# Kernel tuning notes

Hardware: AMD Instinct MI355X
Metric: run time of the kernel (lower is better)

Reference implementation:

```python
import jax, jax.numpy as jnp
import numpy as np

SCALE_FACTOR = 8.0  # sqrt(head_dim=64)
GAMMA = 1.0
NEG_INF = -1e9


def setup_inputs() -> dict:
    key = jax.random.key(0)
    kq, kk, kv, km = jax.random.split(key, 4)
    B, H, S, D = 4, 16, 2048, 64
    q = jax.random.normal(kq, (B, H, S, D), dtype=jnp.float32)
    k = jax.random.normal(kk, (B, H, S, D), dtype=jnp.float32)
    v = jax.random.normal(kv, (B, H, S, D), dtype=jnp.float32)
    mask = jax.random.randint(km, (B, 1, S, S), 0, 2, dtype=jnp.int32)
    return {"q": q, "k": k, "v": v, "mask": mask}


def reference(q, k, v, mask):
    # attn = (q/scale) @ k^T, masked, softmax along last dim, scaled by gamma
    scores = jnp.einsum("bhsd,bhtd->bhst", q / SCALE_FACTOR, k)  # [B,H,S,S]
    scores = jnp.where(mask == 0, NEG_INF, scores)
    attn = jax.nn.softmax(scores, axis=-1) * GAMMA
    output = jnp.einsum("bhst,bhtd->bhsd", attn, v) + v  # AV + residual V
    return (output, attn)
```

## Files before the change

kernel.cpp:

```cpp
#include <hip/hip_runtime.h>

typedef _Float16 f16;
typedef _Float16 f16x4 __attribute__((ext_vector_type(4)));
typedef _Float16 f16x8 __attribute__((ext_vector_type(8)));
typedef float f32x16 __attribute__((ext_vector_type(16)));

#define MFMA16(a, b, c) __builtin_amdgcn_mfma_f32_32x32x16_f16((a), (b), (c), 0, 0, 0)

constexpr int B_ = 4, H_ = 16, S_ = 2048, D_ = 64, BH = 64;
constexpr int QB = 128;
constexpr int WQ = 32;
constexpr int KB = 64;
constexpr int TS = 512;
constexpr int NSPLIT = S_ / TS;
constexpr int NKT_W = TS / KB;
constexpr int NKT = S_ / KB;
constexpr int MW = S_ / 32;
constexpr size_t OUT0 = (size_t)B_ * H_ * S_ * D_;
constexpr size_t WS_RSUM_OFF = (size_t)B_ * S_ * MW;

__device__ __forceinline__ int swzb(int row, int col ) {
  int byte = (row << 7) + (col << 1);
  return byte ^ ((row & 7) << 4);
}

__device__ __forceinline__ void kload256(const float* g, int kt, int tid, float4 kr[4]) {
#pragma unroll
  for (int rep = 0; rep < 4; ++rep) {
    int idx = (rep * 256 + tid) * 4;
    kr[rep] = *(const float4*)(g + (size_t)(kt * KB + (idx >> 6)) * D_ + (idx & 63));
  }
}
__device__ __forceinline__ void kwrite256(char* KlB, int tid, const float4 kr[4]) {
#pragma unroll
  for (int rep = 0; rep < 4; ++rep) {
    int idx = (rep * 256 + tid) * 4;
    f16x4 hx = {(f16)kr[rep].x, (f16)kr[rep].y, (f16)kr[rep].z, (f16)kr[rep].w};
    *(f16x4*)(KlB + swzb(idx >> 6, idx & 63)) = hx;
  }
}
__device__ __forceinline__ void vwrite256(char* VtB, int tid, const float4 vr[4]) {
#pragma unroll
  for (int rep = 0; rep < 4; ++rep) {
    int idx = (rep * 256 + tid) * 4;
    int row = idx >> 6, col = idx & 63;
    *(f16*)(VtB + swzb(col + 0, row)) = (f16)vr[rep].x;
    *(f16*)(VtB + swzb(col + 1, row)) = (f16)vr[rep].y;
    *(f16*)(VtB + swzb(col + 2, row)) = (f16)vr[rep].z;
    *(f16*)(VtB + swzb(col + 3, row)) = (f16)vr[rep].w;
  }
}

__device__ __forceinline__ void load_qf(const float* qg, int qrow, int hi, f16x8 qf[4]) {
  const float* qr = qg + (size_t)qrow * D_;
#pragma unroll
  for (int s = 0; s < 4; ++s) {
    const int d0 = s * 16 + hi * 8;
    float4 a = *(const float4*)(qr + d0);
    float4 c = *(const float4*)(qr + d0 + 4);
    f16x8 t;
    t[0] = (f16)(a.x * 0.125f); t[1] = (f16)(a.y * 0.125f);
    t[2] = (f16)(a.z * 0.125f); t[3] = (f16)(a.w * 0.125f);
    t[4] = (f16)(c.x * 0.125f); t[5] = (f16)(c.y * 0.125f);
    t[6] = (f16)(c.z * 0.125f); t[7] = (f16)(c.w * 0.125f);
    qf[s] = t;
  }
}

__device__ __forceinline__ f32x16 qk8(const char* KlB, const f16x8 qf[4], int sub, int ln, int hi) {
  f32x16 s;
#pragma unroll
  for (int i = 0; i < 16; ++i) s[i] = 0.0f;
#pragma unroll
  for (int t = 0; t < 4; ++t) {
    f16x8 kf = *(const f16x8*)(KlB + swzb(sub * 32 + ln, t * 16 + hi * 8));
    s = MFMA16(qf[t], kf, s);
  }
  return s;
}

__global__ void zero_ws(float* __restrict__ p, int n) {
  int i = blockIdx.x * blockDim.x + threadIdx.x;
  if (i < n) p[i] = 0.0f;
}

__global__ __launch_bounds__(256) void mask_pack(const int* __restrict__ mg,
                                                 unsigned* __restrict__ mb) {
  const int tid = threadIdx.x, lane = tid & 63, wid = tid >> 6;
  const int row = blockIdx.x * 4 + wid;
  const int* mrow = mg + (size_t)row * S_;
  unsigned long long myw = 0;
#pragma unroll
  for (int w = 0; w < 32; ++w) {
    int m = mrow[w * 64 + lane];
    unsigned long long bal = __ballot(m != 0);
    if (lane == w) myw = bal;
  }
  if (lane < 32) *(unsigned long long*)(mb + (size_t)row * MW + 2 * lane) = myw;
}

__global__ __launch_bounds__(256, 4) void attn_rsum(
    const float* __restrict__ qg_, const float* __restrict__ kg_,
    const unsigned* __restrict__ mb, float* __restrict__ ws) {
  __shared__ f16 Kl[KB * D_];
  const int tid = threadIdx.x, lane = tid & 63, wid = tid >> 6;
  const int ln = lane & 31, hi = lane >> 5;
  const int i = blockIdx.x;
  const int work = (i & 7) * 512 + (i >> 3);
  const int bh = work >> 6, rem = work & 63;
  const int qb = (rem & 15) * QB + wid * WQ;
  const int kt0 = (rem >> 4) * NKT_W;
  const int b = bh >> 4;
  const float* qg = qg_ + (size_t)bh * S_ * D_;
  const float* kg = kg_ + (size_t)bh * S_ * D_;
  const unsigned* mbB = mb + (size_t)b * S_ * MW;
  char* KlB = (char*)Kl;

  f16x8 qf[4];
  load_qf(qg, qb + ln, hi, qf);
  float rs[16];
#pragma unroll
  for (int r = 0; r < 16; ++r) rs[r] = 0.0f;

  float4 kr[4];
  kload256(kg, kt0, tid, kr);
  for (int it = 0; it < NKT_W; ++it) {
    __syncthreads();
    kwrite256(KlB, tid, kr);
    if (it + 1 < NKT_W) kload256(kg, kt0 + it + 1, tid, kr);
    __syncthreads();
#pragma unroll
    for (int sub = 0; sub < 2; ++sub) {
      const int t0 = (kt0 + it) * KB + sub * 32;
      f32x16 sacc = qk8(KlB, qf, sub, ln, hi);
#pragma unroll
      for (int r = 0; r < 16; ++r) {
        const int qoff = (r & 3) + 8 * (r >> 2);
        const unsigned mw = mbB[(size_t)(qb + qoff + 4 * hi) * MW + (t0 >> 5)];
        rs[r] += ((mw >> ln) & 1u) ? __expf(sacc[r]) : 0.0f;
      }
    }
  }
  float* wsrow = ws + (size_t)bh * S_;
#pragma unroll
  for (int r = 0; r < 16; ++r) {
    float s = rs[r];
    s += __shfl_xor(s, 16); s += __shfl_xor(s, 8); s += __shfl_xor(s, 4);
    s += __shfl_xor(s, 2); s += __shfl_xor(s, 1);
    if (ln == 0) {
      const int qoff = (r & 3) + 8 * (r >> 2);
      atomicAdd(wsrow + qb + qoff + 4 * hi, s);
    }
  }
}

__global__ __launch_bounds__(256, 4) void attn_emit(
    const float* __restrict__ qg_, const float* __restrict__ kg_,
    const unsigned* __restrict__ mb, const float* __restrict__ ws,
    float* __restrict__ out) {
  __shared__ f16 Kl[KB * D_];
  const int tid = threadIdx.x, lane = tid & 63, wid = tid >> 6;
  const int ln = lane & 31, hi = lane >> 5;
  const int i = blockIdx.x;
  const int work = (i & 7) * 512 + (i >> 3);
  const int bh = work >> 6, rem = work & 63;
  const int qb = (rem & 15) * QB + wid * WQ;
  const int kt0 = (rem >> 4) * NKT_W;
  const int b = bh >> 4;
  const float* qg = qg_ + (size_t)bh * S_ * D_;
  const float* kg = kg_ + (size_t)bh * S_ * D_;
  const unsigned* mbB = mb + (size_t)b * S_ * MW;
  float* attnp = out + OUT0 + (size_t)bh * S_ * S_;
  char* KlB = (char*)Kl;

  f16x8 qf[4];
  load_qf(qg, qb + ln, hi, qf);
  const float* wsrow = ws + (size_t)bh * S_;
  float rinv[16];
#pragma unroll
  for (int r = 0; r < 16; ++r) {
    const int qoff = (r & 3) + 8 * (r >> 2);
    rinv[r] = 1.0f / wsrow[qb + qoff + 4 * hi];
  }

  float4 kr[4];
  kload256(kg, kt0, tid, kr);
  for (int it = 0; it < NKT_W; ++it) {
    __syncthreads();
    kwrite256(KlB, tid, kr);
    if (it + 1 < NKT_W) kload256(kg, kt0 + it + 1, tid, kr);
    __syncthreads();
#pragma unroll
    for (int sub = 0; sub < 2; ++sub) {
      const int t0 = (kt0 + it) * KB + sub * 32;
      f32x16 sacc = qk8(KlB, qf, sub, ln, hi);
      float* arow = attnp + (size_t)(qb + 4 * hi) * S_ + t0 + ln;
#pragma unroll
      for (int r = 0; r < 16; ++r) {
        const int qoff = (r & 3) + 8 * (r >> 2);
        const unsigned mw = mbB[(size_t)(qb + qoff + 4 * hi) * MW + (t0 >> 5)];
        float p = ((mw >> ln) & 1u) ? __expf(sacc[r]) * rinv[r] : 0.0f;
        arow[(size_t)qoff * S_] = p;
      }
    }
  }
}

__global__ __launch_bounds__(256) void attn_out(
    const float* __restrict__ qg_, const float* __restrict__ kg_,
    const float* __restrict__ vg_, const unsigned* __restrict__ mb,
    const float* __restrict__ ws, float* __restrict__ out) {
  __shared__ f16 Kl[KB * D_];
  __shared__ f16 Vt[D_ * KB];
  __shared__ f16 Pl[4 * WQ * KB];
  const int tid = threadIdx.x, lane = tid & 63, wid = tid >> 6;
  const int ln = lane & 31, hi = lane >> 5;
  const int i = blockIdx.x;
  const int work = (i & 7) * 128 + (i >> 3);
  const int bh = work >> 4;
  const int qb = (work & 15) * QB + wid * WQ;
  const int b = bh >> 4;
  const float* qg = qg_ + (size_t)bh * S_ * D_;
  const float* kg = kg_ + (size_t)bh * S_ * D_;
  const float* vg = vg_ + (size_t)bh * S_ * D_;
  const unsigned* mbB = mb + (size_t)b * S_ * MW;
  float* outp = out + (size_t)bh * S_ * D_;
  char* KlB = (char*)Kl;
  char* VtB = (char*)Vt;
  char* PlB = (char*)Pl + wid * (WQ * KB * 2);

  f16x8 qf[4];
  load_qf(qg, qb + ln, hi, qf);
  const float* wsrow = ws + (size_t)bh * S_;
  float rinv[16];
#pragma unroll
  for (int r = 0; r < 16; ++r) {
    const int qoff = (r & 3) + 8 * (r >> 2);
    rinv[r] = 1.0f / wsrow[qb + qoff + 4 * hi];
  }

  f32x16 oacc0, oacc1;
#pragma unroll
  for (int i2 = 0; i2 < 16; ++i2) { oacc0[i2] = 0.0f; oacc1[i2] = 0.0f; }

  float4 kr[4], vr[4];
  kload256(kg, 0, tid, kr);
  kload256(vg, 0, tid, vr);
  for (int kt = 0; kt < NKT; ++kt) {
    __syncthreads();
    kwrite256(KlB, tid, kr);
    vwrite256(VtB, tid, vr);
    if (kt + 1 < NKT) {
      kload256(kg, kt + 1, tid, kr);
      kload256(vg, kt + 1, tid, vr);
    }
    __syncthreads();
#pragma unroll
    for (int sub = 0; sub < 2; ++sub) {
      const int t0 = kt * KB + sub * 32;
      f32x16 sacc = qk8(KlB, qf, sub, ln, hi);
#pragma unroll
      for (int r = 0; r < 16; ++r) {
        const int qoff = (r & 3) + 8 * (r >> 2);
        const unsigned mw = mbB[(size_t)(qb + qoff + 4 * hi) * MW + (t0 >> 5)];
        float p = ((mw >> ln) & 1u) ? __expf(sacc[r]) * rinv[r] : 0.0f;
        *(f16*)(PlB + swzb(qoff + 4 * hi, sub * 32 + ln)) = (f16)p;
      }
    }
#pragma unroll
    for (int ts = 0; ts < 4; ++ts) {
      f16x8 pa = *(const f16x8*)(PlB + swzb(ln, ts * 16 + hi * 8));
      f16x8 vb0 = *(const f16x8*)(VtB + swzb(ln, ts * 16 + hi * 8));
      f16x8 vb1 = *(const f16x8*)(VtB + swzb(32 + ln, ts * 16 + hi * 8));
      oacc0 = MFMA16(pa, vb0, oacc0);
      oacc1 = MFMA16(pa, vb1, oacc1);
    }
  }

#pragma unroll
  for (int r = 0; r < 16; ++r) {
    const int qoff = (r & 3) + 8 * (r >> 2);
    const size_t o = (size_t)(qb + qoff + 4 * hi) * D_ + ln;
    outp[o] = oacc0[r] + vg[o];
    outp[o + 32] = oacc1[r] + vg[o + 32];
  }
}

extern "C" void kernel_launch(void* const* d_in, const int* in_sizes, int n_in,
                              void* d_out, int out_size, void* d_ws, size_t ws_size,
                              hipStream_t stream) {
  (void)in_sizes; (void)n_in; (void)out_size; (void)ws_size;
  const float* q = (const float*)d_in[0];
  const float* k = (const float*)d_in[1];
  const float* v = (const float*)d_in[2];
  const int* mask = (const int*)d_in[3];
  float* out = (float*)d_out;
  unsigned* mb = (unsigned*)d_ws;
  float* rs = (float*)d_ws + WS_RSUM_OFF;

  const int nsum = BH * S_;
  zero_ws<<<dim3((nsum + 255) / 256), dim3(256), 0, stream>>>(rs, nsum);
  mask_pack<<<dim3(B_ * S_ / 4), dim3(256), 0, stream>>>(mask, mb);
  attn_rsum<<<dim3(16 * NSPLIT * BH), dim3(256), 0, stream>>>(q, k, mb, rs);
  attn_emit<<<dim3(16 * NSPLIT * BH), dim3(256), 0, stream>>>(q, k, mb, rs, out);
  attn_out<<<dim3(16 * BH), dim3(256), 0, stream>>>(q, k, v, mb, rs, out);
}
```

Baseline: 1.937 ms.

## Double-buffer K/V shared tiles, halve key split, fold zeroing into mask_pack

All three attention kernels now hold two shared-memory K tiles (and two V tiles in attn_out). The next tile is written into the idle buffer while the current one is consumed, which cuts the barriers per iteration from two to one and overlaps LDS stores with MFMA work. The key-range split for the row-sum and emit kernels shrinks from 512 to 256 keys, doubling the block count for more parallelism at the cost of more atomics and a larger per-block prologue. The separate workspace-zeroing kernel is merged into mask_pack to save a launch. The doubled LDS footprint may reduce occupancy.

```diff
diff --git a/kernel.cpp b/kernel.cpp
--- a/kernel.cpp
+++ b/kernel.cpp
@@ -11,7 +11,8 @@
 constexpr int QB = 128;
 constexpr int WQ = 32;
 constexpr int KB = 64;
-constexpr int TS = 512;
+constexpr int TILE_B = KB * D_ * 2;
+constexpr int TS = 256;
 constexpr int NSPLIT = S_ / TS;
 constexpr int NKT_W = TS / KB;
 constexpr int NKT = S_ / KB;
@@ -67,26 +68,24 @@
   }
 }
 
-__device__ __forceinline__ f32x16 qk8(const char* KlB, const f16x8 qf[4], int sub, int ln, int hi) {
+__device__ __forceinline__ f32x16 qk8(const char* Kc, const f16x8 qf[4], int sub, int ln, int hi) {
   f32x16 s;
 #pragma unroll
   for (int i = 0; i < 16; ++i) s[i] = 0.0f;
 #pragma unroll
   for (int t = 0; t < 4; ++t) {
-    f16x8 kf = *(const f16x8*)(KlB + swzb(sub * 32 + ln, t * 16 + hi * 8));
+    f16x8 kf = *(const f16x8*)(Kc + swzb(sub * 32 + ln, t * 16 + hi * 8));
     s = MFMA16(qf[t], kf, s);
   }
   return s;
 }
 
-__global__ void zero_ws(float* __restrict__ p, int n) {
-  int i = blockIdx.x * blockDim.x + threadIdx.x;
-  if (i < n) p[i] = 0.0f;
-}
-
 __global__ __launch_bounds__(256) void mask_pack(const int* __restrict__ mg,
-                                                 unsigned* __restrict__ mb) {
+                                                 unsigned* __restrict__ mb,
+                                                 float* __restrict__ rs) {
   const int tid = threadIdx.x, lane = tid & 63, wid = tid >> 6;
+  const int gid = blockIdx.x * 256 + tid;
+  if (gid < BH * S_) rs[gid] = 0.0f;
   const int row = blockIdx.x * 4 + wid;
   const int* mrow = mg + (size_t)row * S_;
   unsigned long long myw = 0;
@@ -102,12 +101,12 @@
 __global__ __launch_bounds__(256, 4) void attn_rsum(
     const float* __restrict__ qg_, const float* __restrict__ kg_,
     const unsigned* __restrict__ mb, float* __restrict__ ws) {
-  __shared__ f16 Kl[KB * D_];
+  __shared__ f16 Kl[2 * KB * D_];
   const int tid = threadIdx.x, lane = tid & 63, wid = tid >> 6;
   const int ln = lane & 31, hi = lane >> 5;
   const int i = blockIdx.x;
-  const int work = (i & 7) * 512 + (i >> 3);
-  const int bh = work >> 6, rem = work & 63;
+  const int work = (i & 7) * 1024 + (i >> 3);
+  const int bh = work >> 7, rem = work & 127;
   const int qb = (rem & 15) * QB + wid * WQ;
   const int kt0 = (rem >> 4) * NKT_W;
   const int b = bh >> 4;
@@ -118,33 +117,39 @@
 
   f16x8 qf[4];
   load_qf(qg, qb + ln, hi, qf);
-  float rs[16];
-#pragma unroll
-  for (int r = 0; r < 16; ++r) rs[r] = 0.0f;
+  float rsum[16];
+#pragma unroll
+  for (int r = 0; r < 16; ++r) rsum[r] = 0.0f;
 
   float4 kr[4];
   kload256(kg, kt0, tid, kr);
+  kwrite256(KlB, tid, kr);
+  kload256(kg, kt0 + 1, tid, kr);
+  __syncthreads();
   for (int it = 0; it < NKT_W; ++it) {
-    __syncthreads();
-    kwrite256(KlB, tid, kr);
-    if (it + 1 < NKT_W) kload256(kg, kt0 + it + 1, tid, kr);
-    __syncthreads();
+    const int cur = it & 1;
+    if (it + 1 < NKT_W) {
+      kwrite256(KlB + (cur ^ 1) * TILE_B, tid, kr);
+      if (it + 2 < NKT_W) kload256(kg, kt0 + it + 2, tid, kr);
+    }
+    const char* Kc = KlB + cur * TILE_B;
 #pragma unroll
     for (int sub = 0; sub < 2; ++sub) {
       const int t0 = (kt0 + it) * KB + sub * 32;
-      f32x16 sacc = qk8(KlB, qf, sub, ln, hi);
+      f32x16 sacc = qk8(Kc, qf, sub, ln, hi);
 #pragma unroll
       for (int r = 0; r < 16; ++r) {
         const int qoff = (r & 3) + 8 * (r >> 2);
         const unsigned mw = mbB[(size_t)(qb + qoff + 4 * hi) * MW + (t0 >> 5)];
-        rs[r] += ((mw >> ln) & 1u) ? __expf(sacc[r]) : 0.0f;
+        rsum[r] += ((mw >> ln) & 1u) ? __expf(sacc[r]) : 0.0f;
       }
     }
+    __syncthreads();
   }
   float* wsrow = ws + (size_t)bh * S_;
 #pragma unroll
   for (int r = 0; r < 16; ++r) {
-    float s = rs[r];
+    float s = rsum[r];
     s += __shfl_xor(s, 16); s += __shfl_xor(s, 8); s += __shfl_xor(s, 4);
     s += __shfl_xor(s, 2); s += __shfl_xor(s, 1);
     if (ln == 0) {
@@ -158,12 +163,12 @@
     const float* __restrict__ qg_, const float* __restrict__ kg_,
     const unsigned* __restrict__ mb, const float* __restrict__ ws,
     float* __restrict__ out) {
-  __shared__ f16 Kl[KB * D_];
+  __shared__ f16 Kl[2 * KB * D_];
   const int tid = threadIdx.x, lane = tid & 63, wid = tid >> 6;
   const int ln = lane & 31, hi = lane >> 5;
   const int i = blockIdx.x;
-  const int work = (i & 7) * 512 + (i >> 3);
-  const int bh = work >> 6, rem = work & 63;
+  const int work = (i & 7) * 1024 + (i >> 3);
+  const int bh = work >> 7, rem = work & 127;
   const int qb = (rem & 15) * QB + wid * WQ;
   const int kt0 = (rem >> 4) * NKT_W;
   const int b = bh >> 4;
@@ -185,15 +190,20 @@
 
   float4 kr[4];
   kload256(kg, kt0, tid, kr);
+  kwrite256(KlB, tid, kr);
+  kload256(kg, kt0 + 1, tid, kr);
+  __syncthreads();
   for (int it = 0; it < NKT_W; ++it) {
-    __syncthreads();
-    kwrite256(KlB, tid, kr);
-    if (it + 1 < NKT_W) kload256(kg, kt0 + it + 1, tid, kr);
-    __syncthreads();
+    const int cur = it & 1;
+    if (it + 1 < NKT_W) {
+      kwrite256(KlB + (cur ^ 1) * TILE_B, tid, kr);
+      if (it + 2 < NKT_W) kload256(kg, kt0 + it + 2, tid, kr);
+    }
+    const char* Kc = KlB + cur * TILE_B;
 #pragma unroll
     for (int sub = 0; sub < 2; ++sub) {
       const int t0 = (kt0 + it) * KB + sub * 32;
-      f32x16 sacc = qk8(KlB, qf, sub, ln, hi);
+      f32x16 sacc = qk8(Kc, qf, sub, ln, hi);
       float* arow = attnp + (size_t)(qb + 4 * hi) * S_ + t0 + ln;
 #pragma unroll
       for (int r = 0; r < 16; ++r) {
@@ -203,6 +213,7 @@
         arow[(size_t)qoff * S_] = p;
       }
     }
+    __syncthreads();
   }
 }
 
@@ -210,8 +221,8 @@
     const float* __restrict__ qg_, const float* __restrict__ kg_,
     const float* __restrict__ vg_, const unsigned* __restrict__ mb,
     const float* __restrict__ ws, float* __restrict__ out) {
-  __shared__ f16 Kl[KB * D_];
-  __shared__ f16 Vt[D_ * KB];
+  __shared__ f16 Kl[2 * KB * D_];
+  __shared__ f16 Vt[2 * D_ * KB];
   __shared__ f16 Pl[4 * WQ * KB];
   const int tid = threadIdx.x, lane = tid & 63, wid = tid >> 6;
   const int ln = lane & 31, hi = lane >> 5;
@@ -246,19 +257,27 @@
   float4 kr[4], vr[4];
   kload256(kg, 0, tid, kr);
   kload256(vg, 0, tid, vr);
+  kwrite256(KlB, tid, kr);
+  vwrite256(VtB, tid, vr);
+  kload256(kg, 1, tid, kr);
+  kload256(vg, 1, tid, vr);
+  __syncthreads();
   for (int kt = 0; kt < NKT; ++kt) {
-    __syncthreads();
-    kwrite256(KlB, tid, kr);
-    vwrite256(VtB, tid, vr);
+    const int cur = kt & 1;
     if (kt + 1 < NKT) {
-      kload256(kg, kt + 1, tid, kr);
-      kload256(vg, kt + 1, tid, vr);
-    }
-    __syncthreads();
+      kwrite256(KlB + (cur ^ 1) * TILE_B, tid, kr);
+      vwrite256(VtB + (cur ^ 1) * TILE_B, tid, vr);
+      if (kt + 2 < NKT) {
+        kload256(kg, kt + 2, tid, kr);
+        kload256(vg, kt + 2, tid, vr);
+      }
+    }
+    const char* Kc = KlB + cur * TILE_B;
+    const char* Vc = VtB + cur * TILE_B;
 #pragma unroll
     for (int sub = 0; sub < 2; ++sub) {
       const int t0 = kt * KB + sub * 32;
-      f32x16 sacc = qk8(KlB, qf, sub, ln, hi);
+      f32x16 sacc = qk8(Kc, qf, sub, ln, hi);
 #pragma unroll
       for (int r = 0; r < 16; ++r) {
         const int qoff = (r & 3) + 8 * (r >> 2);
@@ -270,11 +289,12 @@
 #pragma unroll
     for (int ts = 0; ts < 4; ++ts) {
       f16x8 pa = *(const f16x8*)(PlB + swzb(ln, ts * 16 + hi * 8));
-      f16x8 vb0 = *(const f16x8*)(VtB + swzb(ln, ts * 16 + hi * 8));
-      f16x8 vb1 = *(const f16x8*)(VtB + swzb(32 + ln, ts * 16 + hi * 8));
+      f16x8 vb0 = *(const f16x8*)(Vc + swzb(ln, ts * 16 + hi * 8));
+      f16x8 vb1 = *(const f16x8*)(Vc + swzb(32 + ln, ts * 16 + hi * 8));
       oacc0 = MFMA16(pa, vb0, oacc0);
       oacc1 = MFMA16(pa, vb1, oacc1);
     }
+    __syncthreads();
   }
 
 #pragma unroll
@@ -298,9 +318,7 @@
   unsigned* mb = (unsigned*)d_ws;
   float* rs = (float*)d_ws + WS_RSUM_OFF;
 
-  const int nsum = BH * S_;
-  zero_ws<<<dim3((nsum + 255) / 256), dim3(256), 0, stream>>>(rs, nsum);
-  mask_pack<<<dim3(B_ * S_ / 4), dim3(256), 0, stream>>>(mask, mb);
+  mask_pack<<<dim3(B_ * S_ / 4), dim3(256), 0, stream>>>(mask, mb, rs);
   attn_rsum<<<dim3(16 * NSPLIT * BH), dim3(256), 0, stream>>>(q, k, mb, rs);
   attn_emit<<<dim3(16 * NSPLIT * BH), dim3(256), 0, stream>>>(q, k, mb, rs, out);
   attn_out<<<dim3(16 * BH), dim3(256), 0, stream>>>(q, k, v, mb, rs, out);
```

Result: slower. 2.023 ms (+4.4%).
